# Optimization experiments

Measured on AMD Instinct MI355X. Metric: run time of the kernel, lower is better.

The kernel has to match this reference:

```python
import jax, jax.numpy as jnp
import numpy as np

N = 16384

def setup_inputs() -> dict:
    key = jax.random.key(0)
    k1, k2, k3 = jax.random.split(key, 3)
    risk_scores = jax.random.normal(k1, (N,), dtype=jnp.float32)
    survival_times = jax.random.normal(k2, (N,), dtype=jnp.float32)
    # 0/1 event indicator (1 = event observed, 0 = censored)
    events = (jax.random.uniform(k3, (N,)) < 0.5).astype(jnp.float32)
    return {"risk_scores": risk_scores, "survival_times": survival_times, "events": events}

def reference(risk_scores, survival_times, events):
    # Risk-set matrix: R[i, j] = 1 if T[j] >= T[i] (vectorized version of the
    # original O(n^2) double Python loop).
    R = (survival_times[None, :] >= survival_times[:, None]).astype(risk_scores.dtype)  # [n, n]
    exp_theta = jnp.exp(risk_scores)                # [n]
    # sum_j exp(theta_j) * R[i, j]  ->  matvec
    risk_set_sum = R @ exp_theta                    # [n]
    loss = -jnp.mean((risk_scores - jnp.log(risk_set_sum)) * events)
    return loss
```

## Files before the change

kernel.cpp:

```cpp
#include <hip/hip_runtime.h>
#include <math.h>

#define NF 16384
#define NB 4096
#define TPB 256
#define NBLK (NF/TPB)
#define CHUNK (NB/TPB)
#define NMETA (3*NB+1)
#define BLOCK 256

__device__ __forceinline__ int bucket_of(float t) {
    int b = (int)((t + 6.0f) * (NB / 12.0f));
    return min(max(b, 0), NB - 1);
}

__global__ __launch_bounds__(TPB) void surv_hist(
        const float* __restrict__ theta, const float* __restrict__ T,
        float* __restrict__ Earr, int* __restrict__ cnt, float* __restrict__ hE) {
    const int i = blockIdx.x * TPB + threadIdx.x;
    const float Tv = T[i];
    const float Ev = expf(theta[i]);
    Earr[i] = Ev;
    const int b = bucket_of(Tv);
    atomicAdd(&cnt[b], 1);
    atomicAdd(&hE[b], Ev);
}

__global__ __launch_bounds__(TPB) void surv_scan_scatter(
        const float* __restrict__ T, const float* __restrict__ Earr,
        const int* __restrict__ cnt, const float* __restrict__ hE,
        int* __restrict__ rel, int* __restrict__ pfxg, float* __restrict__ sfxg,
        float2* __restrict__ sorted) {
    __shared__ int   pfx[NB + 1];
    __shared__ float sfx[NB];
    __shared__ int   sc[TPB];
    __shared__ float se[TPB];

    const int tid  = threadIdx.x;
    const int base = tid * CHUNK;

    int lc[CHUNK]; float le[CHUNK];
    int cs = 0; float es = 0.f;
    #pragma unroll
    for (int k = 0; k < CHUNK; ++k) {
        lc[k] = cnt[base + k];
        le[k] = hE[base + k];
        cs += lc[k]; es += le[k];
    }
    sc[tid] = cs; se[tid] = es;
    __syncthreads();
    for (int s = 1; s < TPB; s <<= 1) {
        int   a = (tid >= s)      ? sc[tid - s] : 0;
        float f = (tid + s < TPB) ? se[tid + s] : 0.f;
        __syncthreads();
        sc[tid] += a; se[tid] += f;
        __syncthreads();
    }
    {   int run = sc[tid] - cs;
        #pragma unroll
        for (int k = 0; k < CHUNK; ++k) { pfx[base + k] = run; run += lc[k]; }
        if (tid == TPB - 1) pfx[NB] = run;
    }
    {   float rs = se[tid] - es;
        #pragma unroll
        for (int k = CHUNK - 1; k >= 0; --k) { sfx[base + k] = rs; rs += le[k]; }
    }
    __syncthreads();

    if (blockIdx.x == 0) {
        for (int idx = tid; idx < NB + 1; idx += TPB) pfxg[idx] = pfx[idx];
        for (int idx = tid; idx < NB;     idx += TPB) sfxg[idx] = sfx[idx];
    }

    const int i = blockIdx.x * TPB + tid;
    const float Tv = T[i];
    const float Ev = Earr[i];
    const int b = bucket_of(Tv);
    const int pos = pfx[b] + atomicAdd(&rel[b], 1);
    sorted[pos] = make_float2(Tv, Ev);
}

__global__ __launch_bounds__(TPB) void surv_risk(
        const float* __restrict__ theta, const float* __restrict__ T,
        const float* __restrict__ events,
        const int* __restrict__ pfxg, const float* __restrict__ sfxg,
        const float2* __restrict__ sorted,
        float* __restrict__ bsum, int* __restrict__ ticket,
        float* __restrict__ out) {
    __shared__ float ws4[TPB / 64];
    __shared__ int last;

    const int tid = threadIdx.x;
    const int i = blockIdx.x * TPB + tid;
    const float Tv = T[i];
    const int b = bucket_of(Tv);
    float r = sfxg[b];
    const int p1 = pfxg[b + 1];
    for (int p = pfxg[b]; p < p1; ++p) {
        float2 v = sorted[p];
        r += (v.x >= Tv) ? v.y : 0.f;
    }
    float term = (theta[i] - logf(r)) * events[i];

    #pragma unroll
    for (int off = 32; off > 0; off >>= 1) term += __shfl_down(term, off, 64);
    if ((tid & 63) == 0) ws4[tid >> 6] = term;
    __syncthreads();
    if (tid == 0) {
        bsum[blockIdx.x] = ws4[0] + ws4[1] + ws4[2] + ws4[3];
        __threadfence();
        last = (atomicAdd(ticket, 1) == NBLK - 1) ? 1 : 0;
    }
    __syncthreads();
    if (last && tid < 64) {
        float v = atomicAdd(&bsum[tid], 0.f);
        #pragma unroll
        for (int off = 32; off > 0; off >>= 1) v += __shfl_down(v, off, 64);
        if (tid == 0) out[0] = -v / (float)NF;
    }
}

__global__ void surv_partial_bf(const float* __restrict__ theta, const float* __restrict__ T,
                                const float* __restrict__ events, float* __restrict__ bsum, int n) {
    __shared__ float red[BLOCK];
    const int tid = threadIdx.x;
    const int i = blockIdx.x * BLOCK + tid;
    float term = 0.f;
    if (i < n) {
        const float Ti = T[i];
        float risk = 0.f;
        for (int j = 0; j < n; ++j)
            risk += (T[j] >= Ti) ? expf(theta[j]) : 0.f;
        term = (theta[i] - logf(risk)) * events[i];
    }
    red[tid] = term;
    __syncthreads();
    for (int s = BLOCK / 2; s > 0; s >>= 1) {
        if (tid < s) red[tid] += red[tid + s];
        __syncthreads();
    }
    if (tid == 0) bsum[blockIdx.x] = red[0];
}

__global__ void surv_final(const float* __restrict__ bsum, float* __restrict__ out,
                           int nblocks, int n) {
    float v = 0.f;
    for (int b = threadIdx.x; b < nblocks; b += 64) v += bsum[b];
    for (int off = 32; off > 0; off >>= 1) v += __shfl_down(v, off, 64);
    if (threadIdx.x == 0) out[0] = -v / (float)n;
}

extern "C" void kernel_launch(void* const* d_in, const int* in_sizes, int n_in,
                              void* d_out, int out_size, void* d_ws, size_t ws_size,
                              hipStream_t stream) {
    const float* theta  = (const float*)d_in[0];
    const float* T      = (const float*)d_in[1];
    const float* events = (const float*)d_in[2];
    float* out = (float*)d_out;
    const int n = in_sizes[0];

    const size_t need = ((size_t)3 * NF + (NB + 1) + NB + NBLK + NMETA) * 4;
    const bool fast = (n == NF) && ((size_t)ws_size >= need);

    if (!fast) {
        const int nbi = (n + BLOCK - 1) / BLOCK;
        float* bsum = (float*)d_ws;
        surv_partial_bf<<<nbi, BLOCK, 0, stream>>>(theta, T, events, bsum, n);
        surv_final<<<1, 64, 0, stream>>>(bsum, out, nbi, n);
        return;
    }

    float2* sorted = (float2*)d_ws;
    float*  Earr   = (float*)d_ws + 2 * NF;
    int*    pfxg   = (int*)(Earr + NF);
    float*  sfxg   = (float*)(pfxg + NB + 1);
    float*  bsum   = sfxg + NB;
    int*    meta   = (int*)(bsum + NBLK);
    int*    cnt    = meta;
    float*  hE     = (float*)(meta + NB);
    int*    rel    = meta + 2 * NB;
    int*    ticket = meta + 3 * NB;

    hipMemsetAsync(meta, 0, (size_t)NMETA * 4, stream);
    surv_hist<<<NBLK, TPB, 0, stream>>>(theta, T, Earr, cnt, hE);
    surv_scan_scatter<<<NBLK, TPB, 0, stream>>>(T, Earr, cnt, hE, rel,
                                                pfxg, sfxg, sorted);
    surv_risk<<<NBLK, TPB, 0, stream>>>(theta, T, events, pfxg, sfxg, sorted,
                                        bsum, ticket, out);
}
```

Baseline: 83.32 us.

## Replace global-atomic histogram with per-block shared histograms and deterministic scatter

The histogram kernel now builds per-block bucket counts and exp-sums with shared-memory atomics and records each element's rank within its bucket. It writes these per-block slabs to the workspace. The scan kernel reduces all slabs to get global prefix/suffix sums and per-block offsets, so elements can be scattered without global atomics. This removes the memset launch and global atomic contention, and the bucket count is halved. The cost is that every scan block re-reads all slabs, and buckets become larger, which lengthens the per-element in-bucket scan in the risk kernel.

```diff
diff --git a/kernel.cpp b/kernel.cpp
--- a/kernel.cpp
+++ b/kernel.cpp
@@ -2,11 +2,10 @@
 #include <math.h>
 
 #define NF 16384
-#define NB 4096
+#define NB 2048
 #define TPB 256
 #define NBLK (NF/TPB)
-#define CHUNK (NB/TPB)
-#define NMETA (3*NB+1)
+#define PBK (NB/TPB)
 #define BLOCK 256
 
 __device__ __forceinline__ int bucket_of(float t) {
@@ -16,68 +15,98 @@
 
 __global__ __launch_bounds__(TPB) void surv_hist(
         const float* __restrict__ theta, const float* __restrict__ T,
-        float* __restrict__ Earr, int* __restrict__ cnt, float* __restrict__ hE) {
-    const int i = blockIdx.x * TPB + threadIdx.x;
+        float* __restrict__ Earr, int* __restrict__ rank,
+        int* __restrict__ slabC, float* __restrict__ slabE,
+        int* __restrict__ ticket) {
+    __shared__ int   lc[NB];
+    __shared__ float le[NB];
+    const int tid = threadIdx.x;
+    const int g   = blockIdx.x;
+
+    #pragma unroll
+    for (int k = 0; k < PBK; ++k) { lc[tid + k * TPB] = 0; le[tid + k * TPB] = 0.f; }
+    __syncthreads();
+
+    const int i = g * TPB + tid;
     const float Tv = T[i];
     const float Ev = expf(theta[i]);
+    const int b = bucket_of(Tv);
     Earr[i] = Ev;
-    const int b = bucket_of(Tv);
-    atomicAdd(&cnt[b], 1);
-    atomicAdd(&hE[b], Ev);
+    rank[i] = atomicAdd(&lc[b], 1);
+    atomicAdd(&le[b], Ev);
+    __syncthreads();
+
+    #pragma unroll
+    for (int k = 0; k < PBK; ++k) {
+        slabC[g * NB + tid + k * TPB] = lc[tid + k * TPB];
+        slabE[g * NB + tid + k * TPB] = le[tid + k * TPB];
+    }
+    if (g == 0 && tid == 0) *ticket = 0;
 }
 
 __global__ __launch_bounds__(TPB) void surv_scan_scatter(
         const float* __restrict__ T, const float* __restrict__ Earr,
-        const int* __restrict__ cnt, const float* __restrict__ hE,
-        int* __restrict__ rel, int* __restrict__ pfxg, float* __restrict__ sfxg,
+        const int* __restrict__ rank,
+        const int* __restrict__ slabC, const float* __restrict__ slabE,
+        int* __restrict__ pfxg, float* __restrict__ sfxg,
         float2* __restrict__ sorted) {
-    __shared__ int   pfx[NB + 1];
+    __shared__ int   pfx[NB];
+    __shared__ int   offg[NB];
     __shared__ float sfx[NB];
     __shared__ int   sc[TPB];
     __shared__ float se[TPB];
 
     const int tid  = threadIdx.x;
-    const int base = tid * CHUNK;
-
-    int lc[CHUNK]; float le[CHUNK];
+    const int g    = blockIdx.x;
+    const int base = tid * PBK;
+
+    int ct[PBK]; float et[PBK]; int og[PBK];
+    #pragma unroll
+    for (int k = 0; k < PBK; ++k) { ct[k] = 0; et[k] = 0.f; og[k] = 0; }
+    for (int s = 0; s < NBLK; ++s) {
+        #pragma unroll
+        for (int k = 0; k < PBK; ++k) {
+            const int   c = slabC[s * NB + base + k];
+            const float e = slabE[s * NB + base + k];
+            if (s == g) og[k] = ct[k];
+            ct[k] += c; et[k] += e;
+        }
+    }
     int cs = 0; float es = 0.f;
     #pragma unroll
-    for (int k = 0; k < CHUNK; ++k) {
-        lc[k] = cnt[base + k];
-        le[k] = hE[base + k];
-        cs += lc[k]; es += le[k];
-    }
+    for (int k = 0; k < PBK; ++k) { cs += ct[k]; es += et[k]; }
     sc[tid] = cs; se[tid] = es;
     __syncthreads();
     for (int s = 1; s < TPB; s <<= 1) {
-        int   a = (tid >= s)      ? sc[tid - s] : 0;
-        float f = (tid + s < TPB) ? se[tid + s] : 0.f;
+        const int   a = (tid >= s)      ? sc[tid - s] : 0;
+        const float f = (tid + s < TPB) ? se[tid + s] : 0.f;
         __syncthreads();
         sc[tid] += a; se[tid] += f;
         __syncthreads();
     }
     {   int run = sc[tid] - cs;
         #pragma unroll
-        for (int k = 0; k < CHUNK; ++k) { pfx[base + k] = run; run += lc[k]; }
-        if (tid == TPB - 1) pfx[NB] = run;
+        for (int k = 0; k < PBK; ++k) {
+            pfx[base + k] = run; offg[base + k] = og[k]; run += ct[k];
+        }
     }
     {   float rs = se[tid] - es;
         #pragma unroll
-        for (int k = CHUNK - 1; k >= 0; --k) { sfx[base + k] = rs; rs += le[k]; }
-    }
-    __syncthreads();
-
-    if (blockIdx.x == 0) {
-        for (int idx = tid; idx < NB + 1; idx += TPB) pfxg[idx] = pfx[idx];
-        for (int idx = tid; idx < NB;     idx += TPB) sfxg[idx] = sfx[idx];
-    }
-
-    const int i = blockIdx.x * TPB + tid;
+        for (int k = PBK - 1; k >= 0; --k) { sfx[base + k] = rs; rs += et[k]; }
+    }
+    __syncthreads();
+
+    if (g == 0) {
+        for (int idx = tid; idx < NB; idx += TPB) {
+            pfxg[idx] = pfx[idx]; sfxg[idx] = sfx[idx];
+        }
+        if (tid == 0) pfxg[NB] = NF;
+    }
+
+    const int i = g * TPB + tid;
     const float Tv = T[i];
-    const float Ev = Earr[i];
     const int b = bucket_of(Tv);
-    const int pos = pfx[b] + atomicAdd(&rel[b], 1);
-    sorted[pos] = make_float2(Tv, Ev);
+    sorted[pfx[b] + offg[b] + rank[i]] = make_float2(Tv, Earr[i]);
 }
 
 __global__ __launch_bounds__(TPB) void surv_risk(
@@ -97,7 +126,7 @@
     float r = sfxg[b];
     const int p1 = pfxg[b + 1];
     for (int p = pfxg[b]; p < p1; ++p) {
-        float2 v = sorted[p];
+        const float2 v = sorted[p];
         r += (v.x >= Tv) ? v.y : 0.f;
     }
     float term = (theta[i] - logf(r)) * events[i];
@@ -159,7 +188,8 @@
     float* out = (float*)d_out;
     const int n = in_sizes[0];
 
-    const size_t need = ((size_t)3 * NF + (NB + 1) + NB + NBLK + NMETA) * 4;
+    const size_t need = ((size_t)2 * NBLK * NB + 2 * NF + (NB + 1) + NB
+                         + 2 * NF + NBLK + 1) * 4;
     const bool fast = (n == NF) && ((size_t)ws_size >= need);
 
     if (!fast) {
@@ -170,20 +200,18 @@
         return;
     }
 
-    float2* sorted = (float2*)d_ws;
-    float*  Earr   = (float*)d_ws + 2 * NF;
-    int*    pfxg   = (int*)(Earr + NF);
+    int*    slabC  = (int*)d_ws;
+    float*  slabE  = (float*)(slabC + (size_t)NBLK * NB);
+    float*  Earr   = slabE + (size_t)NBLK * NB;
+    int*    rank   = (int*)(Earr + NF);
+    int*    pfxg   = rank + NF;
     float*  sfxg   = (float*)(pfxg + NB + 1);
-    float*  bsum   = sfxg + NB;
-    int*    meta   = (int*)(bsum + NBLK);
-    int*    cnt    = meta;
-    float*  hE     = (float*)(meta + NB);
-    int*    rel    = meta + 2 * NB;
-    int*    ticket = meta + 3 * NB;
-
-    hipMemsetAsync(meta, 0, (size_t)NMETA * 4, stream);
-    surv_hist<<<NBLK, TPB, 0, stream>>>(theta, T, Earr, cnt, hE);
-    surv_scan_scatter<<<NBLK, TPB, 0, stream>>>(T, Earr, cnt, hE, rel,
+    float2* sorted = (float2*)(sfxg + NB);
+    float*  bsum   = (float*)(sorted + NF);
+    int*    ticket = (int*)(bsum + NBLK);
+
+    surv_hist<<<NBLK, TPB, 0, stream>>>(theta, T, Earr, rank, slabC, slabE, ticket);
+    surv_scan_scatter<<<NBLK, TPB, 0, stream>>>(T, Earr, rank, slabC, slabE,
                                                 pfxg, sfxg, sorted);
     surv_risk<<<NBLK, TPB, 0, stream>>>(theta, T, events, pfxg, sfxg, sorted,
                                         bsum, ticket, out);
```

New measurement: 93.79 us. +12.6%, slower.
